# Kernel tuning notes

Measured on AMD Instinct MI355X. Metric: run time of the kernel, lower is better.

The kernel has to match this reference:

```python
import jax, jax.numpy as jnp
import numpy as np

TOP_K = 10
EPS = 1e-8


def setup_inputs() -> dict:
    key = jax.random.key(0)
    k1, k2, k3 = jax.random.split(key, 3)
    N, D = 8192, 1024
    return {
        "image_features": jax.random.normal(k1, (N, D), dtype=jnp.float32),
        "text_features": jax.random.normal(k2, (N, D), dtype=jnp.float32),
        "logit_scale": jnp.asarray(100.0, dtype=jnp.float32),
        "img_index": jax.random.randint(k3, (N,), 0, 1000, dtype=jnp.int64),
    }


def _soft_labels(text_features, img_index):
    # cosine similarity matrix (replaces the blocked double loop; same math)
    norms = jnp.linalg.norm(text_features, axis=1, keepdims=True)
    tn = text_features / jnp.maximum(norms, EPS)
    sim = tn @ tn.T                                  # (N, N)
    N = sim.shape[0]
    eye = jnp.eye(N, dtype=sim.dtype)
    # topk over sim with diagonal zeroed (matches fill_diagonal_(0) on a clone)
    k = min(TOP_K, N)
    _, idx = jax.lax.top_k(sim * (1.0 - eye), k)     # (N, k)
    rows = jnp.arange(N)[:, None]
    mask_sim = jnp.zeros_like(sim).at[rows, idx].set(1.0)
    mask_sim = jnp.where(eye > 0, 1.0, mask_sim)     # fill_diagonal_(1)
    mask_class = (img_index[:, None] == img_index[None, :]).astype(sim.dtype)
    s = sim * mask_sim * mask_class
    return s / jnp.sum(s, axis=1, keepdims=True)     # row-normalized soft labels


def reference(image_features, text_features, logit_scale, img_index):
    logits_per_image = logit_scale * (image_features @ text_features.T)
    logits_per_text = logit_scale * (text_features @ image_features.T)
    labels = _soft_labels(text_features, img_index)  # computed under no_grad in torch
    ce_i = jnp.mean(-jnp.sum(labels * jax.nn.log_softmax(logits_per_image, axis=-1), axis=-1))
    ce_t = jnp.mean(-jnp.sum(labels * jax.nn.log_softmax(logits_per_text, axis=-1), axis=-1))
    return (ce_i + ce_t) / 2
```

## Files before the change

### kernel.cpp

```cpp
#include <hip/hip_runtime.h>
#include <stdint.h>

#define N_ROWS 8192
#define D_DIM  1024
#define TOPK   10
#define NCLS   1000
#define CAND_MAX 32

typedef __attribute__((ext_vector_type(8))) short  s8v;
typedef __attribute__((ext_vector_type(4))) short  s4v;
typedef __attribute__((ext_vector_type(4))) float  f4v;
typedef __attribute__((ext_vector_type(4))) int    i4v;
typedef __attribute__((ext_vector_type(8))) int    i8v;
typedef unsigned long long u64;
typedef unsigned int       u32;
typedef unsigned char      u8;

static __device__ __forceinline__ short f2bf(float f) {
    union { float f; u32 u; } v; v.f = f;
    u32 u = v.u;
    u32 r = (u + 0x7fffu + ((u >> 16) & 1u)) >> 16;
    return (short)r;
}
static __device__ __forceinline__ float bf2f(short s) {
    union { float f; u32 u; } v;
    v.u = ((u32)(unsigned short)s) << 16;
    return v.f;
}

#if defined(__has_builtin)
#if __has_builtin(__builtin_amdgcn_cvt_pk_fp8_f32)
#define HAVE_CVT_FP8 1
#endif
#endif

static __device__ __forceinline__ u8 f2e4m3_sw(float x) {
    u32 u = __float_as_uint(x);
    u32 s = (u >> 24) & 0x80u;
    u32 a = u & 0x7fffffffu;
    if (a >= 0x43e00000u) return (u8)(s | 0x7e);
    if (a < 0x3c800000u) {
        float q = fabsf(x) * 512.0f;
        int n = (int)rintf(q);
        return (u8)(s | (u32)n);
    }
    u32 r = a + 0x0007ffffu + ((a >> 20) & 1u);
    u32 E = (r >> 23) - 127u + 7u;
    return (u8)(s | (E << 3) | ((r >> 20) & 7u));
}

static __device__ __forceinline__ u32 pack4_fp8(float f0, float f1, float f2, float f3) {
#ifdef HAVE_CVT_FP8
    u32 w = (u32)__builtin_amdgcn_cvt_pk_fp8_f32(f0, f1, 0, false);
    w = (u32)__builtin_amdgcn_cvt_pk_fp8_f32(f2, f3, (int)w, true);
    return w;
#else
    return (u32)f2e4m3_sw(f0) | ((u32)f2e4m3_sw(f1) << 8) |
           ((u32)f2e4m3_sw(f2) << 16) | ((u32)f2e4m3_sw(f3) << 24);
#endif
}

static __device__ __forceinline__ void BAR() {
    asm volatile("" ::: "memory");
    __builtin_amdgcn_s_barrier();
    asm volatile("" ::: "memory");
}

static __device__ __forceinline__ u64 packkey(float v, int idx) {
    u32 u = __float_as_uint(v);
    u = (u & 0x80000000u) ? ~u : (u | 0x80000000u);
    return ((u64)u << 32) | (u32)idx;
}

__global__ __launch_bounds__(256) void prep_kernel(
    const float* __restrict__ img, const float* __restrict__ txt,
    short* __restrict__ img_b, short* __restrict__ txt_b, short* __restrict__ tn_b,
    u32* __restrict__ img8, u32* __restrict__ txt8, u32* __restrict__ tn8)
{
    const int row = blockIdx.x;
    const int tid = threadIdx.x;
    const size_t base = (size_t)row * D_DIM + tid * 4;
    f4v tv = *(const f4v*)(txt + base);
    f4v iv = *(const f4v*)(img + base);
    float ss = tv[0]*tv[0] + tv[1]*tv[1] + tv[2]*tv[2] + tv[3]*tv[3];
    #pragma unroll
    for (int m = 32; m >= 1; m >>= 1) ss += __shfl_xor(ss, m);
    __shared__ float red4[4];
    if ((tid & 63) == 0) red4[tid >> 6] = ss;
    __syncthreads();
    float tot = red4[0] + red4[1] + red4[2] + red4[3];
    float inv = 1.0f / fmaxf(sqrtf(tot), 1e-8f);
    s4v tb, nb, ib;
    #pragma unroll
    for (int j = 0; j < 4; ++j) {
        tb[j] = f2bf(tv[j]);
        nb[j] = f2bf(tv[j] * inv);
        ib[j] = f2bf(iv[j]);
    }
    *(s4v*)(txt_b + base) = tb;
    *(s4v*)(tn_b  + base) = nb;
    *(s4v*)(img_b + base) = ib;
    const size_t wbase = (size_t)row * (D_DIM / 4) + tid;
    img8[wbase] = pack4_fp8(iv[0], iv[1], iv[2], iv[3]);
    txt8[wbase] = pack4_fp8(tv[0], tv[1], tv[2], tv[3]);
    tn8[wbase]  = pack4_fp8(tv[0]*inv, tv[1]*inv, tv[2]*inv, tv[3]*inv);
}

__global__ void detect_idx_kernel(const int* __restrict__ idx32, int* __restrict__ flag)
{
    int i = blockIdx.x * blockDim.x + threadIdx.x;
    if (idx32[2 * i + 1] != 0) atomicOr(flag, 1);
}

__global__ __launch_bounds__(256) void hist_kernel(const int* __restrict__ idx32,
    const int* __restrict__ flag, int* __restrict__ hist)
{
    const int i = blockIdx.x * 256 + threadIdx.x;
    const int is64 = (flag[0] == 0);
    const int c = is64 ? idx32[2 * i] : idx32[i];
    atomicAdd(&hist[c], 1);
}

__global__ void prefix_kernel(const int* __restrict__ hist, int* __restrict__ starts)
{
    const int lane = threadIdx.x;
    int acc = 0;
    for (int base = 0; base < NCLS; base += 64) {
        int v = (base + lane < NCLS) ? hist[base + lane] : 0;
        int p = v;
        #pragma unroll
        for (int s = 1; s < 64; s <<= 1) {
            int o = __shfl_up(p, s);
            if (lane >= s) p += o;
        }
        if (base + lane < NCLS) starts[base + lane] = acc + p - v;
        acc += __shfl(p, 63);
    }
    if (lane == 0) starts[NCLS] = acc;
}

__global__ __launch_bounds__(256) void scatter_kernel(const int* __restrict__ idx32,
    const int* __restrict__ flag, const int* __restrict__ starts,
    int* __restrict__ cursor, int* __restrict__ items)
{
    const int i = blockIdx.x * 256 + threadIdx.x;
    const int is64 = (flag[0] == 0);
    const int c = is64 ? idx32[2 * i] : idx32[i];
    const int pos = atomicAdd(&cursor[c], 1);
    items[starts[c] + pos] = i;
}

__global__ __launch_bounds__(256) void cand_kernel(const short* __restrict__ tn,
    const int* __restrict__ idx32, const int* __restrict__ flag,
    const int* __restrict__ starts, const int* __restrict__ items,
    float* __restrict__ candVal, int* __restrict__ candIdx, int* __restrict__ candCnt)
{
    const int lane = threadIdx.x & 63, wid = threadIdx.x >> 6;
    const int i = blockIdx.x * 4 + wid;
    const int is64 = (flag[0] == 0);
    const int c = is64 ? idx32[2 * i] : idx32[i];
    const int s0 = starts[c], s1 = starts[c + 1];
    const short* ai = tn + (size_t)i * D_DIM + lane * 16;
    s8v a0 = *(const s8v*)ai, a1 = *(const s8v*)(ai + 8);
    float af[16];
    #pragma unroll
    for (int e = 0; e < 8; ++e) { af[e] = bf2f(a0[e]); af[8 + e] = bf2f(a1[e]); }
    int out = 0;
    for (int q = s0; q < s1; ++q) {
        int j = items[q];
        if (j == i) continue;
        const short* bj = tn + (size_t)j * D_DIM + lane * 16;
        s8v b0 = *(const s8v*)bj, b1 = *(const s8v*)(bj + 8);
        float s = 0.f;
        #pragma unroll
        for (int e = 0; e < 8; ++e) s += af[e] * bf2f(b0[e]) + af[8 + e] * bf2f(b1[e]);
        #pragma unroll
        for (int m = 1; m < 64; m <<= 1) s += __shfl_xor(s, m);
        if (out < CAND_MAX && lane == 0) {
            candVal[(size_t)i * CAND_MAX + out] = s;
            candIdx[(size_t)i * CAND_MAX + out] = j;
        }
        ++out;
    }
    if (lane == 0) candCnt[i] = out < CAND_MAX ? out : CAND_MAX;
}

__device__ __forceinline__ void stageMX(u8* dstBuf, const u8* __restrict__ g,
                                        int grow0, int k0, int h, int tid)
{
    const int wid = tid >> 6;
    const int row = h * 64 + (tid >> 3);
    const int gch = (tid & 7) ^ ((tid >> 3) & 7);
    const u8* gp = g + (size_t)(grow0 + row) * D_DIM + k0 + gch * 16;
    u8* lp = dstBuf + h * 8192 + wid * 1024;
    __builtin_amdgcn_global_load_lds((const __attribute__((address_space(1))) void*)gp,
                                     (__attribute__((address_space(3))) void*)lp, 16, 0, 0);
}

static __device__ __forceinline__ i8v ds_frag(const u8* buf, int row, int klane)
{
    const u8* rb = buf + (size_t)row * 128;
    const int c0 = (klane * 2)     ^ (row & 7);
    const int c1 = (klane * 2 + 1) ^ (row & 7);
    i4v lo = *(const i4v*)(rb + c0 * 16);
    i4v hi = *(const i4v*)(rb + c1 * 16);
    return __builtin_shufflevector(lo, hi, 0, 1, 2, 3, 4, 5, 6, 7);
}

#define MFSC(m, n, af) \
    acc[m][n] = __builtin_amdgcn_mfma_scale_f32_16x16x128_f8f6f4( \
        af, bF[n], acc[m][n], 0, 0, 0, sc1, 0, sc1)

template<bool LAST>
__device__ __forceinline__ void kiterMX(int kt,
    const u8* __restrict__ A, const u8* __restrict__ B,
    int arow0, int brow0, int tid, int wr, int wc, int rlane, int klane,
    const u8* curA, const u8* curB, u8* nxtA, u8* nxtB,
    f4v (&acc)[4][4], int sc1)
{
    const int k1 = (kt + 1) * 128;
    i8v aF0, aF1;
    i8v bF[4];
    aF0   = ds_frag(curA, wr * 64 + 0 * 16 + rlane, klane);
    aF1   = ds_frag(curA, wr * 64 + 1 * 16 + rlane, klane);
    bF[0] = ds_frag(curB, wc * 64 + 0 * 16 + rlane, klane);
    bF[1] = ds_frag(curB, wc * 64 + 1 * 16 + rlane, klane);
    if (!LAST) {
        stageMX(nxtA, A, arow0, k1, 0, tid);
        stageMX(nxtA, A, arow0, k1, 1, tid);
        stageMX(nxtB, B, brow0, k1, 0, tid);
        stageMX(nxtB, B, brow0, k1, 1, tid);
    }
    BAR();
    __builtin_amdgcn_s_setprio(1);
    MFSC(0, 0, aF0); MFSC(0, 1, aF0); MFSC(1, 0, aF1); MFSC(1, 1, aF1);
    __builtin_amdgcn_s_setprio(0);
    BAR();
    bF[2] = ds_frag(curB, wc * 64 + 2 * 16 + rlane, klane);
    bF[3] = ds_frag(curB, wc * 64 + 3 * 16 + rlane, klane);
    if (!LAST) {
        stageMX(nxtB, B, brow0, k1, 2, tid);
        stageMX(nxtB, B, brow0, k1, 3, tid);
    }
    BAR();
    __builtin_amdgcn_s_setprio(1);
    MFSC(0, 2, aF0); MFSC(0, 3, aF0); MFSC(1, 2, aF1); MFSC(1, 3, aF1);
    __builtin_amdgcn_s_setprio(0);
    BAR();
    aF0 = ds_frag(curA, wr * 64 + 2 * 16 + rlane, klane);
    aF1 = ds_frag(curA, wr * 64 + 3 * 16 + rlane, klane);
    BAR();
    __builtin_amdgcn_s_setprio(1);
    MFSC(2, 2, aF0); MFSC(2, 3, aF0); MFSC(3, 2, aF1); MFSC(3, 3, aF1);
    __builtin_amdgcn_s_setprio(0);
    BAR();
    __builtin_amdgcn_s_setprio(1);
    MFSC(2, 0, aF0); MFSC(2, 1, aF0); MFSC(3, 0, aF1); MFSC(3, 1, aF1);
    __builtin_amdgcn_s_setprio(0);
    if (!LAST) {
        asm volatile("s_waitcnt vmcnt(0)" ::: "memory");
        __builtin_amdgcn_sched_barrier(0);
    }
    BAR();
}

template<int MODE>
__global__ __launch_bounds__(512, 2) void gemm128mx(
    const u8* __restrict__ A, const u8* __restrict__ B,
    float* __restrict__ partTop,
    u64* __restrict__ rowKeys, u64* __restrict__ colKeys)
{
    __shared__ u8 sA[2][16384];
    __shared__ u8 sB[2][32768];

    const int tid   = threadIdx.x;
    const int lane  = tid & 63, wid = tid >> 6;
    const int wr    = wid >> 2, wc = wid & 3;
    const int rlane = lane & 15, klane = lane >> 4;
    const int sc1   = 0x7f7f7f7f;

    const int bid = blockIdx.x;
    int rb, cb;
    if (MODE == 0) {
        const int t = (bid & 7) * 132 + (bid >> 3);
        int c = (int)((sqrtf(4.0f * (float)t + 1.0f) - 1.0f) * 0.5f);
        while ((c + 1) * (c + 2) <= t) ++c;
        while (c * (c + 1) > t) --c;
        cb = c; rb = t - c * (c + 1);
    } else {
        const int x = bid & 7, q = bid >> 3;
        const int chunk = q >> 6, inner = q & 63;
        rb = x * 8 + (inner & 7);
        cb = chunk * 8 + (inner >> 3);
    }
    const int arow0 = rb * 128, brow0 = cb * 256;

    f4v acc[4][4];
    #pragma unroll
    for (int m = 0; m < 4; ++m)
        #pragma unroll
        for (int n = 0; n < 4; ++n)
            acc[m][n] = (f4v){0.f, 0.f, 0.f, 0.f};

    stageMX(&sA[0][0], A, arow0, 0, 0, tid);
    stageMX(&sA[0][0], A, arow0, 0, 1, tid);
    #pragma unroll
    for (int h = 0; h < 4; ++h) stageMX(&sB[0][0], B, brow0, 0, h, tid);
    asm volatile("s_waitcnt vmcnt(0)" ::: "memory");
    __builtin_amdgcn_sched_barrier(0);
    BAR();

    #pragma unroll 1
    for (int kt2 = 0; kt2 < 3; ++kt2) {
        kiterMX<false>(2 * kt2,     A, B, arow0, brow0, tid, wr, wc, rlane, klane,
                       &sA[0][0], &sB[0][0], &sA[1][0], &sB[1][0], acc, sc1);
        kiterMX<false>(2 * kt2 + 1, A, B, arow0, brow0, tid, wr, wc, rlane, klane,
                       &sA[1][0], &sB[1][0], &sA[0][0], &sB[0][0], acc, sc1);
    }
    kiterMX<false>(6, A, B, arow0, brow0, tid, wr, wc, rlane, klane,
                   &sA[0][0], &sB[0][0], &sA[1][0], &sB[1][0], acc, sc1);
    kiterMX<true>(7, A, B, arow0, brow0, tid, wr, wc, rlane, klane,
                  &sA[1][0], &sB[1][0], &sA[0][0], &sB[0][0], acc, sc1);
    __syncthreads();

    if (MODE == 1) {
        #pragma unroll
        for (int m = 0; m < 4; ++m) {
            #pragma unroll
            for (int rr = 0; rr < 4; ++rr) {
                float bv = acc[m][0][rr]; int bn = 0;
                #pragma unroll
                for (int n = 1; n < 4; ++n)
                    if (acc[m][n][rr] > bv) { bv = acc[m][n][rr]; bn = n; }
                u64 key = packkey(bv, cb * 256 + wc * 64 + bn * 16 + rlane);
                #pragma unroll
                for (int s = 1; s < 16; s <<= 1) {
                    u64 o = __shfl_xor(key, s);
                    if (o > key) key = o;
                }
                const u64 k1 = key;
                const int wcol = (int)(u32)k1;
                float bv2 = -INFINITY; int bn2 = 0;
                #pragma unroll
                for (int n = 0; n < 4; ++n) {
                    int gc = cb * 256 + wc * 64 + n * 16 + rlane;
                    if (gc != wcol && acc[m][n][rr] > bv2) { bv2 = acc[m][n][rr]; bn2 = n; }
                }
                u64 key2 = packkey(bv2, cb * 256 + wc * 64 + bn2 * 16 + rlane);
                if ((cb * 256 + wc * 64 + bn2 * 16 + rlane) == wcol) key2 = 0;
                #pragma unroll
                for (int s = 1; s < 16; s <<= 1) {
                    u64 o = __shfl_xor(key2, s);
                    if (o > key2) key2 = o;
                }
                if (rlane == 0) {
                    const int grow = rb * 128 + wr * 64 + m * 16 + klane * 4 + rr;
                    u64* dst = rowKeys + ((size_t)grow * 128 + cb * 4 + wc) * 2;
                    dst[0] = k1; dst[1] = key2;
                }
            }
        }
        #pragma unroll
        for (int n = 0; n < 4; ++n) {
            float bv = -INFINITY; int bi = 0;
            #pragma unroll
            for (int m = 0; m < 4; ++m)
                #pragma unroll
                for (int rr = 0; rr < 4; ++rr)
                    if (acc[m][n][rr] > bv) { bv = acc[m][n][rr]; bi = m * 16 + klane * 4 + rr; }
            u64 key = packkey(bv, rb * 128 + wr * 64 + bi);
            { u64 o = __shfl_xor(key, 16); if (o > key) key = o; }
            { u64 o = __shfl_xor(key, 32); if (o > key) key = o; }
            const u64 k1 = key;
            const int wrow = (int)(u32)k1;
            float bv2 = -INFINITY; int bi2 = -1;
            #pragma unroll
            for (int m = 0; m < 4; ++m)
                #pragma unroll
                for (int rr = 0; rr < 4; ++rr) {
                    int gr = rb * 128 + wr * 64 + m * 16 + klane * 4 + rr;
                    if (gr != wrow && acc[m][n][rr] > bv2) { bv2 = acc[m][n][rr]; bi2 = gr; }
                }
            u64 key2 = (bi2 >= 0) ? packkey(bv2, bi2) : 0;
            { u64 o = __shfl_xor(key2, 16); if (o > key2) key2 = o; }
            { u64 o = __shfl_xor(key2, 32); if (o > key2) key2 = o; }
            if (klane == 0) {
                const int gcol = cb * 256 + wc * 64 + n * 16 + rlane;
                u64* dst = colKeys + ((size_t)gcol * 128 + rb * 2 + wr) * 2;
                dst[0] = k1; dst[1] = key2;
            }
        }
    } else {
        #pragma unroll
        for (int m = 0; m < 4; ++m) {
            #pragma unroll
            for (int rr = 0; rr < 4; ++rr) {
                const int grow = rb * 128 + wr * 64 + m * 16 + klane * 4 + rr;
                float v[4];
                #pragma unroll
                for (int n = 0; n < 4; ++n) {
                    v[n] = acc[m][n][rr];
                    const int gcol = cb * 256 + wc * 64 + n * 16 + rlane;
                    if (gcol == grow) v[n] = 0.0f;
                }
                float t3[3];
                #pragma unroll
                for (int rd = 0; rd < 3; ++rd) {
                    float lm = fmaxf(fmaxf(v[0], v[1]), fmaxf(v[2], v[3]));
                    #pragma unroll
                    for (int s = 1; s < 16; s <<= 1) lm = fmaxf(lm, __shfl_xor(lm, s));
                    t3[rd] = lm;
                    #pragma unroll
                    for (int n = 0; n < 4; ++n) v[n] = (v[n] == lm) ? -INFINITY : v[n];
                }
                if (rlane == 0) {
                    float* dst = partTop + (size_t)grow * 384 + (size_t)(cb * 4 + wc) * 3;
                    dst[0] = t3[0]; dst[1] = t3[1]; dst[2] = t3[2];
                }
            }
        }
        #pragma unroll
        for (int n = 0; n < 4; ++n) {
            const int gcol = cb * 256 + wc * 64 + n * 16 + rlane;
            float vv[16];
            #pragma unroll
            for (int m = 0; m < 4; ++m)
                #pragma unroll
                for (int rr = 0; rr < 4; ++rr) {
                    const int grow = rb * 128 + wr * 64 + m * 16 + klane * 4 + rr;
                    float val = acc[m][n][rr];
                    if (grow == gcol) val = 0.0f;
                    vv[m * 4 + rr] = val;
                }
            float w0 = -INFINITY, w1 = -INFINITY, w2 = -INFINITY;
            #pragma unroll
            for (int rd = 0; rd < 3; ++rd) {
                float lm = vv[0];
                #pragma unroll
                for (int q = 1; q < 16; ++q) lm = fmaxf(lm, vv[q]);
                if (rd == 0) w0 = lm; else if (rd == 1) w1 = lm; else w2 = lm;
                #pragma unroll
                for (int q = 0; q < 16; ++q) vv[q] = (vv[q] == lm) ? -INFINITY : vv[q];
            }
            #pragma unroll
            for (int s = 16; s < 64; s <<= 1) {
                float o0 = __shfl_xor(w0, s), o1 = __shfl_xor(w1, s), o2 = __shfl_xor(w2, s);
                float c6[6] = {w0, w1, w2, o0, o1, o2};
                #pragma unroll
                for (int rd = 0; rd < 3; ++rd) {
                    float lm = c6[0];
                    #pragma unroll
                    for (int q = 1; q < 6; ++q) lm = fmaxf(lm, c6[q]);
                    if (rd == 0) w0 = lm; else if (rd == 1) w1 = lm; else w2 = lm;
                    #pragma unroll
                    for (int q = 0; q < 6; ++q) c6[q] = (c6[q] == lm) ? -INFINITY : c6[q];
                }
            }
            if (klane == 0) {
                float* dst = partTop + (size_t)gcol * 384 + (size_t)(rb * 2 + wr) * 3;
                dst[0] = w0; dst[1] = w1; dst[2] = w2;
            }
        }
    }
}

__global__ __launch_bounds__(256) void merge_top_kernel(const float* __restrict__ partTop,
                                                        float* __restrict__ thr)
{
    const int lane = threadIdx.x & 63, wid = threadIdx.x >> 6;
    const int row = blockIdx.x * 4 + wid;
    const float* p = partTop + (size_t)row * 384 + lane * 6;
    float v[6];
    #pragma unroll
    for (int q = 0; q < 6; ++q) v[q] = p[q];
    float best = -INFINITY;
    #pragma unroll
    for (int r = 0; r < TOPK; ++r) {
        best = v[0];
        #pragma unroll
        for (int q = 1; q < 6; ++q) best = fmaxf(best, v[q]);
        #pragma unroll
        for (int m = 1; m < 64; m <<= 1) best = fmaxf(best, __shfl_xor(best, m));
        #pragma unroll
        for (int q = 0; q < 6; ++q) v[q] = (v[q] == best) ? -INFINITY : v[q];
    }
    if (lane == 0) thr[row] = best;
}

__global__ __launch_bounds__(256) void merge_cand_kernel(const u64* __restrict__ rowKeys,
    const u64* __restrict__ colKeys, int* __restrict__ rowCand, int* __restrict__ colCand)
{
    const int lane = threadIdx.x & 63, wid = threadIdx.x >> 6;
    const int unit = blockIdx.x * 4 + wid;
    const u64* p = (unit < N_ROWS)
        ? rowKeys + (size_t)unit * 256 + lane * 4
        : colKeys + (size_t)(unit - N_ROWS) * 256 + lane * 4;
    int* out = (unit < N_ROWS) ? rowCand + (size_t)unit * 4
                               : colCand + (size_t)(unit - N_ROWS) * 4;
    u64 k[4];
    #pragma unroll
    for (int q = 0; q < 4; ++q) k[q] = p[q];
    int chosen[4];
    #pragma unroll
    for (int r = 0; r < 4; ++r) {
        u64 best = 0;
        #pragma unroll
        for (int q = 0; q < 4; ++q) {
            int c = (int)(u32)k[q];
            bool excl = false;
            for (int e = 0; e < r; ++e) excl |= (c == chosen[e]);
            if (!excl && k[q] > best) best = k[q];
        }
        #pragma unroll
        for (int s = 1; s < 64; s <<= 1) {
            u64 o = __shfl_xor(best, s);
            if (o > best) best = o;
        }
        chosen[r] = (int)(u32)best;
    }
    if (lane == 0) {
        #pragma unroll
        for (int r = 0; r < 4; ++r) out[r] = chosen[r];
    }
}

__global__ __launch_bounds__(256) void finalize_kernel(
    const float* __restrict__ img, const float* __restrict__ txt,
    const short* __restrict__ img_b, const short* __restrict__ txt_b,
    const float* __restrict__ scale_p,
    const float* __restrict__ candVal, const int* __restrict__ candIdx,
    const int* __restrict__ candCnt, const float* __restrict__ thr,
    const int* __restrict__ rowCand, const int* __restrict__ colCand,
    float* __restrict__ contrib)
{
    const int i   = blockIdx.x;
    const int tid = threadIdx.x;
    const int lane = tid & 63, w = tid >> 6;
    __shared__ float ldots[8];
    __shared__ int   sel[20];
    __shared__ float selw[20];
    __shared__ int   s_cnt;
    __shared__ float s_dots[20];
    __shared__ float s_red[4];

    for (int jj = w; jj < 8; jj += 4) {
        const int j = (jj < 4) ? rowCand[(size_t)i * 4 + jj]
                               : colCand[(size_t)i * 4 + (jj - 4)];
        const short* ap = ((jj < 4) ? img_b : txt_b) + (size_t)i * D_DIM + lane * 16;
        const short* bp = ((jj < 4) ? txt_b : img_b) + (size_t)j * D_DIM + lane * 16;
        s8v a0 = *(const s8v*)ap, a1 = *(const s8v*)(ap + 8);
        s8v b0 = *(const s8v*)bp, b1 = *(const s8v*)(bp + 8);
        float s = 0.f;
        #pragma unroll
        for (int e = 0; e < 8; ++e)
            s += bf2f(a0[e]) * bf2f(b0[e]) + bf2f(a1[e]) * bf2f(b1[e]);
        #pragma unroll
        for (int m = 1; m < 64; m <<= 1) s += __shfl_xor(s, m);
        if (lane == 0) ldots[jj] = s;
    }

    if (tid == 0) {
        int c = 1; sel[0] = i; selw[0] = 1.0f;
        const float t = thr[i] - 1e-5f;
        const int cc = candCnt[i];
        for (int q = 0; q < cc && c < 20; ++q) {
            float v = candVal[(size_t)i * CAND_MAX + q];
            if (v >= t) { sel[c] = candIdx[(size_t)i * CAND_MAX + q]; selw[c] = v; ++c; }
        }
        for (int a = 2; a < c; ++a) {
            int ky = sel[a]; float kv = selw[a]; int b = a - 1;
            while (b >= 1 && sel[b] > ky) { sel[b + 1] = sel[b]; selw[b + 1] = selw[b]; --b; }
            sel[b + 1] = ky; selw[b + 1] = kv;
        }
        s_cnt = c;
    }
    __syncthreads();
    const int c = s_cnt;
    const size_t ib = (size_t)i * D_DIM + tid * 4;
    f4v iv = *(const f4v*)(img + ib);
    f4v ti = *(const f4v*)(txt + ib);
    for (int s = 0; s < c; ++s) {
        const int j = sel[s];
        const size_t jb = (size_t)j * D_DIM + tid * 4;
        f4v tj = *(const f4v*)(txt + jb);
        f4v ij = *(const f4v*)(img + jb);
        float d = iv[0]*tj[0] + iv[1]*tj[1] + iv[2]*tj[2] + iv[3]*tj[3]
                + ij[0]*ti[0] + ij[1]*ti[1] + ij[2]*ti[2] + ij[3]*ti[3];
        #pragma unroll
        for (int m = 32; m >= 1; m >>= 1) d += __shfl_xor(d, m);
        if ((tid & 63) == 0) s_red[tid >> 6] = d;
        __syncthreads();
        if (tid == 0) s_dots[s] = s_red[0] + s_red[1] + s_red[2] + s_red[3];
        __syncthreads();
    }
    if (tid == 0) {
        const float sc = scale_p[0];
        float rm = fmaxf(fmaxf(ldots[0], ldots[1]), fmaxf(ldots[2], ldots[3]));
        float rs = 0.f;
        #pragma unroll
        for (int q = 0; q < 4; ++q) rs += __expf(sc * (ldots[q] - rm));
        float rlse = sc * rm + __logf(rs);
        float cm = fmaxf(fmaxf(ldots[4], ldots[5]), fmaxf(ldots[6], ldots[7]));
        float cs = 0.f;
        #pragma unroll
        for (int q = 4; q < 8; ++q) cs += __expf(sc * (ldots[q] - cm));
        float clse = sc * cm + __logf(cs);
        float den = 0.f;
        for (int s = 0; s < c; ++s) den += selw[s];
        float acc = 0.f;
        for (int s = 0; s < c; ++s) acc += (selw[s] / den) * sc * s_dots[s];
        contrib[i] = rlse + clse - acc;
    }
}

__global__ __launch_bounds__(256) void reduce_kernel(
    const float* __restrict__ contrib, float* __restrict__ out)
{
    const int tid = threadIdx.x;
    float s = 0.f;
    for (int i = tid; i < N_ROWS; i += 256) s += contrib[i];
    #pragma unroll
    for (int m = 32; m >= 1; m >>= 1) s += __shfl_xor(s, m);
    __shared__ float r4[4];
    if ((tid & 63) == 0) r4[tid >> 6] = s;
    __syncthreads();
    if (tid == 0) out[0] = (r4[0] + r4[1] + r4[2] + r4[3]) * (0.5f / (float)N_ROWS);
}

extern "C" void kernel_launch(void* const* d_in, const int* in_sizes, int n_in,
                              void* d_out, int out_size, void* d_ws, size_t ws_size,
                              hipStream_t stream)
{
    const float* img     = (const float*)d_in[0];
    const float* txt     = (const float*)d_in[1];
    const float* scale_p = (const float*)d_in[2];
    const int*   idx32   = (const int*)d_in[3];

    char* ws = (char*)d_ws;
    short* img_b   = (short*)ws; ws += (size_t)N_ROWS * D_DIM * 2;
    short* txt_b   = (short*)ws; ws += (size_t)N_ROWS * D_DIM * 2;
    short* tn_b    = (short*)ws; ws += (size_t)N_ROWS * D_DIM * 2;
    u32*   img8    = (u32*)ws;   ws += (size_t)N_ROWS * D_DIM;
    u32*   txt8    = (u32*)ws;   ws += (size_t)N_ROWS * D_DIM;
    u32*   tn8     = (u32*)ws;   ws += (size_t)N_ROWS * D_DIM;
    float* partTop = (float*)ws; ws += (size_t)N_ROWS * 384 * 4;
    u64*   rowKeys = (u64*)ws;   ws += (size_t)N_ROWS * 256 * 8;
    u64*   colKeys = (u64*)ws;   ws += (size_t)N_ROWS * 256 * 8;
    int*   rowCand = (int*)ws;   ws += (size_t)N_ROWS * 4 * 4;
    int*   colCand = (int*)ws;   ws += (size_t)N_ROWS * 4 * 4;
    float* candVal = (float*)ws; ws += (size_t)N_ROWS * CAND_MAX * 4;
    int*   candIdx = (int*)ws;   ws += (size_t)N_ROWS * CAND_MAX * 4;
    int*   candCnt = (int*)ws;   ws += N_ROWS * 4;
    float* thr     = (float*)ws; ws += N_ROWS * 4;
    float* contrib = (float*)ws; ws += N_ROWS * 4;
    int*   hist    = (int*)ws;   ws += 4096;
    int*   starts  = (int*)ws;   ws += 4096;
    int*   cursor  = (int*)ws;   ws += 4096;
    int*   items   = (int*)ws;   ws += N_ROWS * 4;
    int*   flag    = (int*)ws;   ws += 256;
    float* outf    = (float*)d_out;

    hipMemsetAsync(flag, 0, sizeof(int), stream);
    hipMemsetAsync(hist, 0, NCLS * sizeof(int), stream);
    hipMemsetAsync(cursor, 0, NCLS * sizeof(int), stream);

    prep_kernel<<<N_ROWS, 256, 0, stream>>>(img, txt, img_b, txt_b, tn_b,
                                            img8, txt8, tn8);
    detect_idx_kernel<<<16, 256, 0, stream>>>(idx32, flag);
    hist_kernel<<<N_ROWS / 256, 256, 0, stream>>>(idx32, flag, hist);
    prefix_kernel<<<1, 64, 0, stream>>>(hist, starts);
    scatter_kernel<<<N_ROWS / 256, 256, 0, stream>>>(idx32, flag, starts, cursor, items);
    cand_kernel<<<N_ROWS / 4, 256, 0, stream>>>(tn_b, idx32, flag, starts, items,
                                                candVal, candIdx, candCnt);
    gemm128mx<0><<<1056, 512, 0, stream>>>((const u8*)tn8, (const u8*)tn8,
                                           partTop, nullptr, nullptr);
    gemm128mx<1><<<2048, 512, 0, stream>>>((const u8*)img8, (const u8*)txt8,
                                           nullptr, rowKeys, colKeys);
    merge_top_kernel<<<N_ROWS / 4, 256, 0, stream>>>(partTop, thr);
    merge_cand_kernel<<<N_ROWS / 2, 256, 0, stream>>>(rowKeys, colKeys, rowCand, colCand);
    finalize_kernel<<<N_ROWS, 256, 0, stream>>>(img, txt, img_b, txt_b, scale_p,
                                                candVal, candIdx, candCnt, thr,
                                                rowCand, colCand, contrib);
    reduce_kernel<<<1, 256, 0, stream>>>(contrib, outf);
}
```

Baseline: 389.7 us.

## Triple-buffer MX GEMM LDS staging with prefetch distance two

Replaces the double-buffered K loop, which interleaved loads and MFMAs with many barriers, with a three-stage LDS ring buffer. Each step issues global-to-LDS loads two tiles ahead and waits only for the older batch (vmcnt(6)). All fragments are read up front, followed by 16 back-to-back MFMAs, leaving one barrier per step. LDS use per block grows from 96KB to 144KB, which may drop occupancy from 2 blocks per CU to 1 on a 160KB LDS.

```diff
diff --git a/kernel.cpp b/kernel.cpp
--- a/kernel.cpp
+++ b/kernel.cpp
@@ -207,61 +207,45 @@
     return __builtin_shufflevector(lo, hi, 0, 1, 2, 3, 4, 5, 6, 7);
 }
 
-#define MFSC(m, n, af) \
+#define MFSC(m, n) \
     acc[m][n] = __builtin_amdgcn_mfma_scale_f32_16x16x128_f8f6f4( \
-        af, bF[n], acc[m][n], 0, 0, 0, sc1, 0, sc1)
-
-template<bool LAST>
-__device__ __forceinline__ void kiterMX(int kt,
+        aF[m], bF[n], acc[m][n], 0, 0, 0, sc1, 0, sc1)
+
+template<int DRAIN>
+__device__ __forceinline__ void kiterMX(
     const u8* __restrict__ A, const u8* __restrict__ B,
-    int arow0, int brow0, int tid, int wr, int wc, int rlane, int klane,
+    int arow0, int brow0, int k2, int tid, int wr, int wc, int rlane, int klane,
     const u8* curA, const u8* curB, u8* nxtA, u8* nxtB,
     f4v (&acc)[4][4], int sc1)
 {
-    const int k1 = (kt + 1) * 128;
-    i8v aF0, aF1;
-    i8v bF[4];
-    aF0   = ds_frag(curA, wr * 64 + 0 * 16 + rlane, klane);
-    aF1   = ds_frag(curA, wr * 64 + 1 * 16 + rlane, klane);
-    bF[0] = ds_frag(curB, wc * 64 + 0 * 16 + rlane, klane);
-    bF[1] = ds_frag(curB, wc * 64 + 1 * 16 + rlane, klane);
-    if (!LAST) {
-        stageMX(nxtA, A, arow0, k1, 0, tid);
-        stageMX(nxtA, A, arow0, k1, 1, tid);
-        stageMX(nxtB, B, brow0, k1, 0, tid);
-        stageMX(nxtB, B, brow0, k1, 1, tid);
-    }
-    BAR();
+    if (DRAIN == 6) {
+        stageMX(nxtA, A, arow0, k2, 0, tid);
+        stageMX(nxtA, A, arow0, k2, 1, tid);
+        stageMX(nxtB, B, brow0, k2, 0, tid);
+        stageMX(nxtB, B, brow0, k2, 1, tid);
+        stageMX(nxtB, B, brow0, k2, 2, tid);
+        stageMX(nxtB, B, brow0, k2, 3, tid);
+    }
+    i8v aF[4], bF[4];
+    #pragma unroll
+    for (int f = 0; f < 4; ++f) aF[f] = ds_frag(curA, wr * 64 + f * 16 + rlane, klane);
+    #pragma unroll
+    for (int f = 0; f < 4; ++f) bF[f] = ds_frag(curB, wc * 64 + f * 16 + rlane, klane);
     __builtin_amdgcn_s_setprio(1);
-    MFSC(0, 0, aF0); MFSC(0, 1, aF0); MFSC(1, 0, aF1); MFSC(1, 1, aF1);
+    #pragma unroll
+    for (int m = 0; m < 4; ++m) {
+        MFSC(m, 0); MFSC(m, 1); MFSC(m, 2); MFSC(m, 3);
+    }
     __builtin_amdgcn_s_setprio(0);
-    BAR();
-    bF[2] = ds_frag(curB, wc * 64 + 2 * 16 + rlane, klane);
-    bF[3] = ds_frag(curB, wc * 64 + 3 * 16 + rlane, klane);
-    if (!LAST) {
-        stageMX(nxtB, B, brow0, k1, 2, tid);
-        stageMX(nxtB, B, brow0, k1, 3, tid);
-    }
-    BAR();
-    __builtin_amdgcn_s_setprio(1);
-    MFSC(0, 2, aF0); MFSC(0, 3, aF0); MFSC(1, 2, aF1); MFSC(1, 3, aF1);
-    __builtin_amdgcn_s_setprio(0);
-    BAR();
-    aF0 = ds_frag(curA, wr * 64 + 2 * 16 + rlane, klane);
-    aF1 = ds_frag(curA, wr * 64 + 3 * 16 + rlane, klane);
-    BAR();
-    __builtin_amdgcn_s_setprio(1);
-    MFSC(2, 2, aF0); MFSC(2, 3, aF0); MFSC(3, 2, aF1); MFSC(3, 3, aF1);
-    __builtin_amdgcn_s_setprio(0);
-    BAR();
-    __builtin_amdgcn_s_setprio(1);
-    MFSC(2, 0, aF0); MFSC(2, 1, aF0); MFSC(3, 0, aF1); MFSC(3, 1, aF1);
-    __builtin_amdgcn_s_setprio(0);
-    if (!LAST) {
+    if (DRAIN == 6) {
+        asm volatile("s_waitcnt vmcnt(6)" ::: "memory");
+        __builtin_amdgcn_sched_barrier(0);
+        BAR();
+    } else if (DRAIN == 0) {
         asm volatile("s_waitcnt vmcnt(0)" ::: "memory");
         __builtin_amdgcn_sched_barrier(0);
-    }
-    BAR();
+        BAR();
+    }
 }
 
 template<int MODE>
@@ -270,8 +254,8 @@
     float* __restrict__ partTop,
     u64* __restrict__ rowKeys, u64* __restrict__ colKeys)
 {
-    __shared__ u8 sA[2][16384];
-    __shared__ u8 sB[2][32768];
+    __shared__ u8 sA[3][16384];
+    __shared__ u8 sB[3][32768];
 
     const int tid   = threadIdx.x;
     const int lane  = tid & 63, wid = tid >> 6;
@@ -306,21 +290,30 @@
     stageMX(&sA[0][0], A, arow0, 0, 1, tid);
     #pragma unroll
     for (int h = 0; h < 4; ++h) stageMX(&sB[0][0], B, brow0, 0, h, tid);
-    asm volatile("s_waitcnt vmcnt(0)" ::: "memory");
+    stageMX(&sA[1][0], A, arow0, 128, 0, tid);
+    stageMX(&sA[1][0], A, arow0, 128, 1, tid);
+    #pragma unroll
+    for (int h = 0; h < 4; ++h) stageMX(&sB[1][0], B, brow0, 128, h, tid);
+    asm volatile("s_waitcnt vmcnt(6)" ::: "memory");
     __builtin_amdgcn_sched_barrier(0);
     BAR();
 
-    #pragma unroll 1
-    for (int kt2 = 0; kt2 < 3; ++kt2) {
-        kiterMX<false>(2 * kt2,     A, B, arow0, brow0, tid, wr, wc, rlane, klane,
-                       &sA[0][0], &sB[0][0], &sA[1][0], &sB[1][0], acc, sc1);
-        kiterMX<false>(2 * kt2 + 1, A, B, arow0, brow0, tid, wr, wc, rlane, klane,
-                       &sA[1][0], &sB[1][0], &sA[0][0], &sB[0][0], acc, sc1);
-    }
-    kiterMX<false>(6, A, B, arow0, brow0, tid, wr, wc, rlane, klane,
-                   &sA[0][0], &sB[0][0], &sA[1][0], &sB[1][0], acc, sc1);
-    kiterMX<true>(7, A, B, arow0, brow0, tid, wr, wc, rlane, klane,
-                  &sA[1][0], &sB[1][0], &sA[0][0], &sB[0][0], acc, sc1);
+    kiterMX<6>(A, B, arow0, brow0, 2 * 128, tid, wr, wc, rlane, klane,
+               &sA[0][0], &sB[0][0], &sA[2][0], &sB[2][0], acc, sc1);
+    kiterMX<6>(A, B, arow0, brow0, 3 * 128, tid, wr, wc, rlane, klane,
+               &sA[1][0], &sB[1][0], &sA[0][0], &sB[0][0], acc, sc1);
+    kiterMX<6>(A, B, arow0, brow0, 4 * 128, tid, wr, wc, rlane, klane,
+               &sA[2][0], &sB[2][0], &sA[1][0], &sB[1][0], acc, sc1);
+    kiterMX<6>(A, B, arow0, brow0, 5 * 128, tid, wr, wc, rlane, klane,
+               &sA[0][0], &sB[0][0], &sA[2][0], &sB[2][0], acc, sc1);
+    kiterMX<6>(A, B, arow0, brow0, 6 * 128, tid, wr, wc, rlane, klane,
+               &sA[1][0], &sB[1][0], &sA[0][0], &sB[0][0], acc, sc1);
+    kiterMX<6>(A, B, arow0, brow0, 7 * 128, tid, wr, wc, rlane, klane,
+               &sA[2][0], &sB[2][0], &sA[1][0], &sB[1][0], acc, sc1);
+    kiterMX<0>(A, B, arow0, brow0, 0, tid, wr, wc, rlane, klane,
+               &sA[0][0], &sB[0][0], nullptr, nullptr, acc, sc1);
+    kiterMX<-1>(A, B, arow0, brow0, 0, tid, wr, wc, rlane, klane,
+                &sA[1][0], &sB[1][0], nullptr, nullptr, acc, sc1);
     __syncthreads();
 
     if (MODE == 1) {
```

New measurement: 969.7 us. 2.49x slower.
